# Kernel tuning notes

Hardware: AMD Instinct MI355X
Metric: run time of the kernel (lower is better)

The kernel has to match this reference:

```python
import jax, jax.numpy as jnp
import numpy as np

N, E = 100000, 1600000
NFEAT, NHID, NCLASS, NLAYER = 128, 128, 40, 3


def _glorot(key, shape):
    fan_in, fan_out = shape[0], shape[1]
    lim = float(np.sqrt(6.0 / (fan_in + fan_out)))
    return jax.random.uniform(key, shape, jnp.float32, -lim, lim)


def setup_inputs() -> dict:
    key = jax.random.key(0)
    ks = jax.random.split(key, 12)
    x = jax.random.normal(ks[0], (N, NFEAT), jnp.float32)
    src = jax.random.randint(ks[1], (E,), 0, N, jnp.int32)
    dst = jax.random.randint(ks[2], (E,), 0, N, jnp.int32)
    W1 = _glorot(ks[3], (NFEAT, NHID)); b1 = jnp.zeros((NHID,), jnp.float32)
    W2 = _glorot(ks[4], (NHID, NHID)); b2 = jnp.zeros((NHID,), jnp.float32)
    Wg = jnp.stack([_glorot(ks[5 + l], (NHID, NHID)) for l in range(NLAYER)])  # [L,H,H]
    bg = jnp.zeros((NLAYER, NHID), jnp.float32)
    Wc = _glorot(ks[5 + NLAYER], (NHID, NCLASS)); bc = jnp.zeros((NCLASS,), jnp.float32)
    return {"x": x, "src": src, "dst": dst, "W1": W1, "b1": b1, "W2": W2,
            "b2": b2, "Wg": Wg, "bg": bg, "Wc": Wc, "bc": bc}


def _graph_conv(h, src, dst, W, b, out_norm, in_norm):
    # DGL GraphConv norm='both': scale by src out-deg^{-1/2}, sum-aggregate,
    # scale by dst in-deg^{-1/2}, then linear (in_feats == out_feats -> W after agg).
    h = h * out_norm[:, None]
    agg = jax.ops.segment_sum(h[src], dst, num_segments=N)
    return (agg * in_norm[:, None]) @ W + b


def reference(x, src, dst, W1, b1, W2, b2, Wg, bg, Wc, bc):
    ones = jnp.ones((E,), jnp.float32)
    out_deg = jnp.clip(jax.ops.segment_sum(ones, src, num_segments=N), 1.0)
    in_deg = jnp.clip(jax.ops.segment_sum(ones, dst, num_segments=N), 1.0)
    out_norm = jax.lax.rsqrt(out_deg)
    in_norm = jax.lax.rsqrt(in_deg)

    h = x @ W1 + b1            # feature1
    h = h @ W2 + b2            # feature2
    for l in range(NLAYER):    # stacked GraphConv + ReLU (dropout is identity in eval)
        h = _graph_conv(h, src, dst, Wg[l], bg[l], out_norm, in_norm)
        h = jax.nn.relu(h)
    return h @ Wc + bc         # classifier
```

## Files before the change

### kernel.cpp

```cpp
#include <hip/hip_runtime.h>
#include <hip/hip_fp16.h>
#include <cstdint>
#include <cstddef>

constexpr int NN  = 100000;
constexpr int EE  = 1600000;
constexpr int HID = 128;
constexpr int NBUK = (NN + 511) / 512;
constexpr int BLKE = 2048;
constexpr int NBE  = (EE + BLKE - 1) / BLKE;
constexpr int MH   = NBUK * NBE;
constexpr int NSC  = (MH + 1023) / 1024;

typedef float f32x4_t __attribute__((ext_vector_type(4)));
typedef short bf16x8_t __attribute__((ext_vector_type(8)));

static __device__ __forceinline__ short f2bf(float f) {
    union { float f; unsigned u; } x; x.f = f;
    unsigned r = x.u + 0x7FFF + ((x.u >> 16) & 1);
    return (short)(r >> 16);
}
static __device__ __forceinline__ float bf2f(short b) {
    union { unsigned u; float f; } x; x.u = ((unsigned)(unsigned short)b) << 16;
    return x.f;
}

__global__ __launch_bounds__(256) void bh_both_k(const int* __restrict__ src, const int* __restrict__ dst,
                                                 int* __restrict__ bh_d, int* __restrict__ bh_s) {
    __shared__ int hd[NBUK], hs[NBUK];
    int blk = blockIdx.x, t = threadIdx.x;
    for (int i = t; i < NBUK; i += 256) { hd[i] = 0; hs[i] = 0; }
    __syncthreads();
    int e0 = blk * BLKE, e1 = min(e0 + BLKE, EE);
    for (int e = e0 + t; e < e1; e += 256) {
        atomicAdd(&hd[dst[e] >> 9], 1);
        atomicAdd(&hs[src[e] >> 9], 1);
    }
    __syncthreads();
    for (int i = t; i < NBUK; i += 256) {
        bh_d[i * NBE + blk] = hd[i];
        bh_s[i * NBE + blk] = hs[i];
    }
}

__global__ __launch_bounds__(256) void scan_sum_k(const int* __restrict__ in, int* __restrict__ bsum, int n) {
    __shared__ int sc[256];
    int b = blockIdx.x, t = threadIdx.x;
    int base = b * 1024 + t * 4;
    int s = 0;
#pragma unroll
    for (int j = 0; j < 4; j++) { int idx = base + j; s += (idx < n) ? in[idx] : 0; }
    sc[t] = s; __syncthreads();
    for (int off = 128; off > 0; off >>= 1) {
        if (t < off) sc[t] += sc[t + off];
        __syncthreads();
    }
    if (t == 0) bsum[b] = sc[0];
}

__global__ void scan_top_k(const int* __restrict__ bsum, int* __restrict__ boff, int nb) {
    __shared__ int sc[256];
    int t = threadIdx.x;
    int v = (t < nb) ? bsum[t] : 0;
    sc[t] = v; __syncthreads();
    for (int off = 1; off < 256; off <<= 1) {
        int u = (t >= off) ? sc[t - off] : 0;
        __syncthreads();
        sc[t] += u;
        __syncthreads();
    }
    if (t < nb) boff[t] = sc[t] - v;
}

__global__ __launch_bounds__(256) void scan_chunk_k(const int* __restrict__ in, const int* __restrict__ boff,
                                                    int* __restrict__ out, int n) {
    __shared__ int sc[256];
    int b = blockIdx.x, t = threadIdx.x;
    int base = b * 1024 + t * 4;
    int c[4];
#pragma unroll
    for (int j = 0; j < 4; j++) { int idx = base + j; c[j] = (idx < n) ? in[idx] : 0; }
    int s = c[0] + c[1] + c[2] + c[3];
    sc[t] = s; __syncthreads();
    for (int off = 1; off < 256; off <<= 1) {
        int v = (t >= off) ? sc[t - off] : 0;
        __syncthreads();
        sc[t] += v;
        __syncthreads();
    }
    int excl = sc[t] - s + boff[b];
#pragma unroll
    for (int j = 0; j < 4; j++) {
        int idx = base + j;
        if (idx < n) out[idx] = excl;
        excl += c[j];
    }
}

__global__ __launch_bounds__(256) void scatter_both_k(const int* __restrict__ src, const int* __restrict__ dst,
                                                      const int* __restrict__ off_d, const int* __restrict__ off_s,
                                                      int2* __restrict__ pairs, int* __restrict__ ssorted) {
    __shared__ int cd[NBUK], cs[NBUK];
    int blk = blockIdx.x, t = threadIdx.x;
    for (int i = t; i < NBUK; i += 256) {
        cd[i] = off_d[i * NBE + blk];
        cs[i] = off_s[i * NBE + blk];
    }
    __syncthreads();
    int e0 = blk * BLKE, e1 = min(e0 + BLKE, EE);
    for (int e = e0 + t; e < e1; e += 256) {
        int d = dst[e], s = src[e];
        int pd = atomicAdd(&cd[d >> 9], 1);
        pairs[pd] = make_int2(d, s);
        int ps = atomicAdd(&cs[s >> 9], 1);
        ssorted[ps] = s;
    }
}

__global__ __launch_bounds__(256) void bucket_csr_k(const int2* __restrict__ pairs, const int* __restrict__ off_d,
                                                    int* __restrict__ rowptr, int* __restrict__ col,
                                                    float* __restrict__ inorm) {
    __shared__ int hist[512];
    __shared__ int excl[512];
    __shared__ int psum[256];
    int b = blockIdx.x, t = threadIdx.x;
    int base = off_d[b * NBE];
    int endv = (b == NBUK - 1) ? EE : off_d[(b + 1) * NBE];
    hist[t] = 0; hist[t + 256] = 0;
    __syncthreads();
    for (int i = base + t; i < endv; i += 256) atomicAdd(&hist[pairs[i].x & 511], 1);
    __syncthreads();
    int p0 = hist[2 * t], p1 = hist[2 * t + 1];
    int ps = p0 + p1;
    psum[t] = ps; __syncthreads();
    for (int off = 1; off < 256; off <<= 1) {
        int u = (t >= off) ? psum[t - off] : 0;
        __syncthreads();
        psum[t] += u;
        __syncthreads();
    }
    int pex = psum[t] - ps;
    excl[2 * t] = pex; excl[2 * t + 1] = pex + p0;
    __syncthreads();
    int n0 = b * 512;
#pragma unroll
    for (int j = 0; j < 2; j++) {
        int i = 2 * t + j, node = n0 + i;
        if (node < NN) {
            rowptr[node] = base + excl[i];
            int c = hist[i]; if (c < 1) c = 1;
            inorm[node] = rsqrtf((float)c);
        }
    }
    if (b == NBUK - 1 && t == 0) rowptr[NN] = EE;
    __syncthreads();
    for (int i = base + t; i < endv; i += 256) {
        int2 p = pairs[i];
        int pos = base + atomicAdd(&excl[p.x & 511], 1);
        col[pos] = p.y;
    }
}

__global__ __launch_bounds__(256) void bucket_ocnt_k(const int* __restrict__ ssorted, const int* __restrict__ off_s,
                                                     float* __restrict__ onorm) {
    __shared__ int hist[512];
    int b = blockIdx.x, t = threadIdx.x;
    int base = off_s[b * NBE];
    int endv = (b == NBUK - 1) ? EE : off_s[(b + 1) * NBE];
    hist[t] = 0; hist[t + 256] = 0;
    __syncthreads();
    for (int i = base + t; i < endv; i += 256) atomicAdd(&hist[ssorted[i] & 511], 1);
    __syncthreads();
#pragma unroll
    for (int j = 0; j < 2; j++) {
        int i = t + j * 256, node = b * 512 + i;
        if (node < NN) {
            int c = hist[i]; if (c < 1) c = 1;
            onorm[node] = rsqrtf((float)c);
        }
    }
}

__global__ __launch_bounds__(256) void agg_k(const float4* __restrict__ h16, const int* __restrict__ rowptr,
                                             const int* __restrict__ col, float4* __restrict__ out) {
    int w = (int)((blockIdx.x * 256 + threadIdx.x) >> 6);
    if (w >= NN) return;
    int lane = threadIdx.x & 63;
    int q   = lane >> 4;
    int l16 = lane & 15;
    int beg = rowptr[w], end = rowptr[w + 1];
    float acc[8];
#pragma unroll
    for (int j = 0; j < 8; j++) acc[j] = 0.f;

    union HU { float4 f4; __half2 h2[4]; };
    int i = beg + q;
    for (; i + 12 < end; i += 16) {
        int s0 = col[i], s1 = col[i + 4], s2 = col[i + 8], s3 = col[i + 12];
        HU u0, u1, u2, u3;
        u0.f4 = h16[(size_t)s0 * 16 + l16];
        u1.f4 = h16[(size_t)s1 * 16 + l16];
        u2.f4 = h16[(size_t)s2 * 16 + l16];
        u3.f4 = h16[(size_t)s3 * 16 + l16];
#pragma unroll
        for (int p = 0; p < 4; p++) {
            float2 a = __half22float2(u0.h2[p]);
            float2 b = __half22float2(u1.h2[p]);
            float2 c = __half22float2(u2.h2[p]);
            float2 d = __half22float2(u3.h2[p]);
            acc[2 * p]     += (a.x + b.x) + (c.x + d.x);
            acc[2 * p + 1] += (a.y + b.y) + (c.y + d.y);
        }
    }
    for (; i < end; i += 4) {
        int s = col[i];
        HU u; u.f4 = h16[(size_t)s * 16 + l16];
#pragma unroll
        for (int p = 0; p < 4; p++) {
            float2 a = __half22float2(u.h2[p]);
            acc[2 * p]     += a.x;
            acc[2 * p + 1] += a.y;
        }
    }
#pragma unroll
    for (int m = 16; m <= 32; m <<= 1)
#pragma unroll
        for (int j = 0; j < 8; j++) acc[j] += __shfl_xor(acc[j], m);
    if (q == 0) {
        float4 o0, o1;
        o0.x = acc[0]; o0.y = acc[1]; o0.z = acc[2]; o0.w = acc[3];
        o1.x = acc[4]; o1.y = acc[5]; o1.z = acc[6]; o1.w = acc[7];
        out[(size_t)w * 32 + l16 * 2]     = o0;
        out[(size_t)w * 32 + l16 * 2 + 1] = o1;
    }
}

template <int NT, bool RELU, bool INSCALE, bool OUTSCALE, bool OUTHALF>
__global__ __launch_bounds__(256) void mfma_gemm_k(
    const float* __restrict__ in, const float* __restrict__ inscale,
    const float* __restrict__ W, const float* __restrict__ bias,
    void* __restrict__ outp, const float* __restrict__ outscale,
    int nrows, int ncols, int ngroups) {

    __shared__ short Bh[NT * 2048];
    __shared__ short Bl[NT * 2048];

    const int t = threadIdx.x;

    if constexpr (NT == 8) {
        for (int j = 0; j < 16; j++) {
            int fi = (j * 256 + t) * 4;
            int k = fi >> 7, n0 = fi & 127;
            float4 wv = *(const float4*)(W + fi);
            float wa[4] = {wv.x, wv.y, wv.z, wv.w};
#pragma unroll
            for (int c = 0; c < 4; c++) {
                int n = n0 + c;
                int nt = n >> 4, kblk = k >> 5, ksub = k & 31;
                int lane_ = ((ksub >> 3) << 4) | (n & 15);
                int sidx = ((nt * 4 + kblk) * 64 + lane_) * 8 + (ksub & 7);
                short hi = f2bf(wa[c]);
                short lo = f2bf(wa[c] - bf2f(hi));
                Bh[sidx] = hi; Bl[sidx] = lo;
            }
        }
    } else {
        for (int idx = t; idx < 128 * 64; idx += 256) {
            int k = idx >> 6, n = idx & 63;
            if (n < NT * 16) {
                float w = (n < 40) ? W[k * 40 + n] : 0.f;
                int nt = n >> 4, kblk = k >> 5, ksub = k & 31;
                int lane_ = ((ksub >> 3) << 4) | (n & 15);
                int sidx = ((nt * 4 + kblk) * 64 + lane_) * 8 + (ksub & 7);
                short hi = f2bf(w);
                short lo = f2bf(w - bf2f(hi));
                Bh[sidx] = hi; Bl[sidx] = lo;
            }
        }
    }
    __syncthreads();

    const int wave = t >> 6;
    const int lane = t & 63;
    const int m    = lane & 15;
    const int kq   = lane >> 4;

    for (int g = blockIdx.x; g < ngroups; g += gridDim.x) {
        int grow0 = g * 64 + wave * 16;
        int row   = grow0 + m;
        bool rv   = row < nrows;

        bf16x8_t Ah[4], Al[4];
        float s = 1.f;
        if (INSCALE && rv) s = inscale[row];
#pragma unroll
        for (int kb = 0; kb < 4; kb++) {
            const float* ap = in + (size_t)row * 128 + kb * 32 + kq * 8;
            float4 p0, p1;
            if (rv) { p0 = *(const float4*)ap; p1 = *(const float4*)(ap + 4); }
            else    { p0 = make_float4(0,0,0,0); p1 = make_float4(0,0,0,0); }
            float av[8] = {p0.x, p0.y, p0.z, p0.w, p1.x, p1.y, p1.z, p1.w};
#pragma unroll
            for (int j = 0; j < 8; j++) {
                float v = INSCALE ? av[j] * s : av[j];
                short hi = f2bf(v);
                Ah[kb][j] = hi;
                Al[kb][j] = f2bf(v - bf2f(hi));
            }
        }

        int crow0 = grow0 + kq * 4;
        float osr[4];
#pragma unroll
        for (int r = 0; r < 4; r++) {
            int crow = crow0 + r;
            osr[r] = (OUTSCALE && crow < nrows) ? outscale[crow] : 1.f;
        }

#pragma unroll
        for (int nt = 0; nt < NT; nt++) {
            f32x4_t acc = {0.f, 0.f, 0.f, 0.f};
#pragma unroll
            for (int kb = 0; kb < 4; kb++) {
                const bf16x8_t bh = *(const bf16x8_t*)&Bh[((nt * 4 + kb) * 64 + lane) * 8];
                const bf16x8_t bl = *(const bf16x8_t*)&Bl[((nt * 4 + kb) * 64 + lane) * 8];
                acc = __builtin_amdgcn_mfma_f32_16x16x32_bf16(Ah[kb], bh, acc, 0, 0, 0);
                acc = __builtin_amdgcn_mfma_f32_16x16x32_bf16(Al[kb], bh, acc, 0, 0, 0);
                acc = __builtin_amdgcn_mfma_f32_16x16x32_bf16(Ah[kb], bl, acc, 0, 0, 0);
            }
            int ccol = nt * 16 + m;
            bool cv = (NT == 8) ? true : (ccol < ncols);
            float bv = cv ? bias[ccol] : 0.f;
#pragma unroll
            for (int r = 0; r < 4; r++) {
                int crow = crow0 + r;
                if (crow < nrows && cv) {
                    float v = acc[r] + bv;
                    if (RELU) v = fmaxf(v, 0.f);
                    v *= osr[r];
                    if (OUTHALF) ((__half*)outp)[(size_t)crow * ncols + ccol] = __float2half_rn(v);
                    else         ((float*)outp)[(size_t)crow * ncols + ccol] = v;
                }
            }
        }
    }
}

extern "C" void kernel_launch(void* const* d_in, const int* in_sizes, int n_in,
                              void* d_out, int out_size, void* d_ws, size_t ws_size,
                              hipStream_t stream) {
    const float* x   = (const float*)d_in[0];
    const int*   src = (const int*)d_in[1];
    const int*   dst = (const int*)d_in[2];
    const float* W1  = (const float*)d_in[3];
    const float* b1  = (const float*)d_in[4];
    const float* W2  = (const float*)d_in[5];
    const float* b2  = (const float*)d_in[6];
    const float* Wg  = (const float*)d_in[7];
    const float* bg  = (const float*)d_in[8];
    const float* Wc  = (const float*)d_in[9];
    const float* bc  = (const float*)d_in[10];
    float* out = (float*)d_out;

    char* ws = (char*)d_ws;
    size_t off = 0;
    auto alloc = [&](size_t bytes) -> void* {
        void* p = ws + off;
        off += (bytes + 255) & ~(size_t)255;
        return p;
    };
    float*  h0     = (float*)alloc((size_t)NN * HID * 4);
    float*  h1     = (float*)alloc((size_t)NN * HID * 4);
    __half* h16    = (__half*)alloc((size_t)NN * HID * 2);
    float*  onorm  = (float*)alloc((size_t)NN * 4);
    float*  inorm  = (float*)alloc((size_t)NN * 4);
    int*    rowptr = (int*)alloc((size_t)(NN + 1) * 4);
    int*    col    = (int*)alloc((size_t)EE * 4);
    int*    bh_d   = (int*)alloc((size_t)MH * 4);
    int*    bh_s   = (int*)alloc((size_t)MH * 4);
    int*    off_d  = (int*)alloc((size_t)MH * 4);
    int*    off_s  = (int*)alloc((size_t)MH * 4);
    int*    bsum   = (int*)alloc((size_t)NSC * 4);
    int*    boff   = (int*)alloc((size_t)NSC * 4);
    int2*  pairs   = (int2*)h0;
    int*   ssorted = (int*)(h0 + (size_t)EE * 2);

    bh_both_k<<<NBE, 256, 0, stream>>>(src, dst, bh_d, bh_s);
    scan_sum_k<<<NSC, 256, 0, stream>>>(bh_d, bsum, MH);
    scan_top_k<<<1, 256, 0, stream>>>(bsum, boff, NSC);
    scan_chunk_k<<<NSC, 256, 0, stream>>>(bh_d, boff, off_d, MH);
    scan_sum_k<<<NSC, 256, 0, stream>>>(bh_s, bsum, MH);
    scan_top_k<<<1, 256, 0, stream>>>(bsum, boff, NSC);
    scan_chunk_k<<<NSC, 256, 0, stream>>>(bh_s, boff, off_s, MH);
    scatter_both_k<<<NBE, 256, 0, stream>>>(src, dst, off_d, off_s, pairs, ssorted);
    bucket_csr_k<<<NBUK, 256, 0, stream>>>(pairs, off_d, rowptr, col, inorm);
    bucket_ocnt_k<<<NBUK, 256, 0, stream>>>(ssorted, off_s, onorm);

    const int ngroups = (NN + 63) / 64;
    const int ggrid   = 512;

    mfma_gemm_k<8, false, false, false, false><<<ggrid, 256, 0, stream>>>(
        x, nullptr, W1, b1, h0, nullptr, NN, 128, ngroups);
    mfma_gemm_k<8, false, false, true, true><<<ggrid, 256, 0, stream>>>(
        h0, nullptr, W2, b2, h16, onorm, NN, 128, ngroups);
    for (int l = 0; l < 3; l++) {
        agg_k<<<(NN * 64 + 255) / 256, 256, 0, stream>>>(
            (const float4*)h16, rowptr, col, (float4*)h0);
        if (l < 2) {
            mfma_gemm_k<8, true, true, true, true><<<ggrid, 256, 0, stream>>>(
                h0, inorm, Wg + (size_t)l * 128 * 128, bg + (size_t)l * 128, h16, onorm, NN, 128, ngroups);
        } else {
            mfma_gemm_k<8, true, true, false, false><<<ggrid, 256, 0, stream>>>(
                h0, inorm, Wg + (size_t)l * 128 * 128, bg + (size_t)l * 128, h1, nullptr, NN, 128, ngroups);
        }
    }
    mfma_gemm_k<3, false, false, false, false><<<ggrid, 256, 0, stream>>>(
        h1, nullptr, Wc, bc, out, nullptr, NN, 40, ngroups);
}
```

Before: 613.6 us.

## Fold W1·W2 into one GEMM and store pre-split bf16 hi/lo activations

Precomputes W12 = W1·W2 and b12 = b1·W2 + b2 so the two feature layers collapse into a single GEMM over x. Activations are now written as bf16 hi/lo pairs: by a new split kernel for x, by the aggregation kernel, and by the last graph-conv GEMM. The GEMMs therefore read ready-made MFMA operands instead of fp32 and no longer split them per tile. The GEMM is restructured to 512 threads, with each wave holding one column tile of B in registers, and the in-norm scale is applied after accumulation. This trades an extra split pass over x and two-array bf16 storage for half the GEMM input bandwidth and one fewer full GEMM. The split now truncates the hi part instead of rounding it.

New measurement: 727.4 us. +18.5%, slower.

```diff
diff --git a/kernel.cpp b/kernel.cpp
--- a/kernel.cpp
+++ b/kernel.cpp
@@ -14,15 +14,13 @@
 
 typedef float f32x4_t __attribute__((ext_vector_type(4)));
 typedef short bf16x8_t __attribute__((ext_vector_type(8)));
-
-static __device__ __forceinline__ short f2bf(float f) {
-    union { float f; unsigned u; } x; x.f = f;
-    unsigned r = x.u + 0x7FFF + ((x.u >> 16) & 1);
-    return (short)(r >> 16);
-}
-static __device__ __forceinline__ float bf2f(short b) {
-    union { unsigned u; float f; } x; x.u = ((unsigned)(unsigned short)b) << 16;
-    return x.f;
+typedef unsigned short u16x8_t __attribute__((ext_vector_type(8)));
+
+static __device__ __forceinline__ void fsplit(float v, unsigned short& hi, unsigned short& lo) {
+    unsigned u = __float_as_uint(v);
+    hi = (unsigned short)(u >> 16);
+    float r = v - __uint_as_float(u & 0xFFFF0000u);
+    lo = (unsigned short)(__float_as_uint(r) >> 16);
 }
 
 __global__ __launch_bounds__(256) void bh_both_k(const int* __restrict__ src, const int* __restrict__ dst,
@@ -181,8 +179,45 @@
     }
 }
 
+__global__ __launch_bounds__(256) void w12_k(const float* __restrict__ W1, const float* __restrict__ W2,
+                                             float* __restrict__ W12) {
+    int idx = blockIdx.x * 256 + threadIdx.x;
+    int i = idx >> 7, j = idx & 127;
+    float a0 = 0.f, a1 = 0.f, a2 = 0.f, a3 = 0.f;
+    for (int k = 0; k < 128; k += 4) {
+        a0 = fmaf(W1[i * 128 + k],     W2[(k)     * 128 + j], a0);
+        a1 = fmaf(W1[i * 128 + k + 1], W2[(k + 1) * 128 + j], a1);
+        a2 = fmaf(W1[i * 128 + k + 2], W2[(k + 2) * 128 + j], a2);
+        a3 = fmaf(W1[i * 128 + k + 3], W2[(k + 3) * 128 + j], a3);
+    }
+    W12[idx] = (a0 + a1) + (a2 + a3);
+}
+
+__global__ void b12_k(const float* __restrict__ b1, const float* __restrict__ W2,
+                      const float* __restrict__ b2, float* __restrict__ b12) {
+    int j = threadIdx.x;
+    if (j < 128) {
+        float acc = b2[j];
+        for (int k = 0; k < 128; k++) acc = fmaf(b1[k], W2[k * 128 + j], acc);
+        b12[j] = acc;
+    }
+}
+
+__global__ __launch_bounds__(256) void split_k(const float* __restrict__ x, unsigned short* __restrict__ hi,
+                                               unsigned short* __restrict__ lo) {
+    int i0 = (blockIdx.x * 256 + threadIdx.x) * 8;
+    float4 a = *(const float4*)(x + i0), b = *(const float4*)(x + i0 + 4);
+    float v[8] = {a.x, a.y, a.z, a.w, b.x, b.y, b.z, b.w};
+    u16x8_t h, l;
+#pragma unroll
+    for (int j = 0; j < 8; j++) { unsigned short hh, ll; fsplit(v[j], hh, ll); h[j] = hh; l[j] = ll; }
+    *(u16x8_t*)(hi + i0) = h;
+    *(u16x8_t*)(lo + i0) = l;
+}
+
 __global__ __launch_bounds__(256) void agg_k(const float4* __restrict__ h16, const int* __restrict__ rowptr,
-                                             const int* __restrict__ col, float4* __restrict__ out) {
+                                             const int* __restrict__ col,
+                                             unsigned short* __restrict__ ahi, unsigned short* __restrict__ alo) {
     int w = (int)((blockIdx.x * 256 + threadIdx.x) >> 6);
     if (w >= NN) return;
     int lane = threadIdx.x & 63;
@@ -223,123 +258,103 @@
         }
     }
 #pragma unroll
-    for (int m = 16; m <= 32; m <<= 1)
-#pragma unroll
-        for (int j = 0; j < 8; j++) acc[j] += __shfl_xor(acc[j], m);
+    for (int mm = 16; mm <= 32; mm <<= 1)
+#pragma unroll
+        for (int j = 0; j < 8; j++) acc[j] += __shfl_xor(acc[j], mm);
     if (q == 0) {
-        float4 o0, o1;
-        o0.x = acc[0]; o0.y = acc[1]; o0.z = acc[2]; o0.w = acc[3];
-        o1.x = acc[4]; o1.y = acc[5]; o1.z = acc[6]; o1.w = acc[7];
-        out[(size_t)w * 32 + l16 * 2]     = o0;
-        out[(size_t)w * 32 + l16 * 2 + 1] = o1;
-    }
-}
-
-template <int NT, bool RELU, bool INSCALE, bool OUTSCALE, bool OUTHALF>
-__global__ __launch_bounds__(256) void mfma_gemm_k(
-    const float* __restrict__ in, const float* __restrict__ inscale,
-    const float* __restrict__ W, const float* __restrict__ bias,
-    void* __restrict__ outp, const float* __restrict__ outscale,
+        u16x8_t h, l;
+#pragma unroll
+        for (int j = 0; j < 8; j++) { unsigned short hh, ll; fsplit(acc[j], hh, ll); h[j] = hh; l[j] = ll; }
+        *(u16x8_t*)(ahi + (size_t)w * 128 + l16 * 8) = h;
+        *(u16x8_t*)(alo + (size_t)w * 128 + l16 * 8) = l;
+    }
+}
+
+template <int NT, bool RELU, bool INSC, int OM, bool OUTSC>
+__global__ __launch_bounds__(512) void gemm_bs_k(
+    const unsigned short* __restrict__ Ahi, const unsigned short* __restrict__ Alo,
+    const float* __restrict__ insc,
+    const float* __restrict__ W, int wld, const float* __restrict__ bias,
+    void* __restrict__ o1, void* __restrict__ o2, const float* __restrict__ outsc,
     int nrows, int ncols, int ngroups) {
 
     __shared__ short Bh[NT * 2048];
     __shared__ short Bl[NT * 2048];
-
     const int t = threadIdx.x;
-
-    if constexpr (NT == 8) {
-        for (int j = 0; j < 16; j++) {
-            int fi = (j * 256 + t) * 4;
-            int k = fi >> 7, n0 = fi & 127;
-            float4 wv = *(const float4*)(W + fi);
-            float wa[4] = {wv.x, wv.y, wv.z, wv.w};
-#pragma unroll
-            for (int c = 0; c < 4; c++) {
-                int n = n0 + c;
-                int nt = n >> 4, kblk = k >> 5, ksub = k & 31;
-                int lane_ = ((ksub >> 3) << 4) | (n & 15);
-                int sidx = ((nt * 4 + kblk) * 64 + lane_) * 8 + (ksub & 7);
-                short hi = f2bf(wa[c]);
-                short lo = f2bf(wa[c] - bf2f(hi));
-                Bh[sidx] = hi; Bl[sidx] = lo;
+    for (int idx = t; idx < 128 * 128; idx += 512) {
+        int k = idx >> 7, n = idx & 127;
+        if (n < NT * 16) {
+            float wv = (n < ncols) ? W[k * wld + n] : 0.f;
+            unsigned short hh, ll; fsplit(wv, hh, ll);
+            int nt_ = n >> 4, kblk = k >> 5, ksub = k & 31;
+            int lane_ = ((ksub >> 3) << 4) | (n & 15);
+            int sidx = ((nt_ * 4 + kblk) * 64 + lane_) * 8 + (ksub & 7);
+            Bh[sidx] = (short)hh; Bl[sidx] = (short)ll;
+        }
+    }
+    __syncthreads();
+
+    const int wave = t >> 6, lane = t & 63, m = lane & 15, kq = lane >> 4;
+    int nt, rg0, nrg;
+    bool active;
+    if (NT == 8) { nt = wave; rg0 = 0; nrg = 4; active = true; }
+    else         { nt = wave % 3; rg0 = (wave / 3) * 2; nrg = 2; active = wave < 6; }
+    if (!active) return;
+
+    bf16x8_t bh[4], bl[4];
+#pragma unroll
+    for (int kb = 0; kb < 4; kb++) {
+        bh[kb] = *(const bf16x8_t*)&Bh[((nt * 4 + kb) * 64 + lane) * 8];
+        bl[kb] = *(const bf16x8_t*)&Bl[((nt * 4 + kb) * 64 + lane) * 8];
+    }
+    const int ccol = nt * 16 + m;
+    const bool cv = (NT == 8) || (ccol < ncols);
+    const float bv = cv ? bias[ccol] : 0.f;
+
+    for (int g = blockIdx.x; g < ngroups; g += gridDim.x) {
+        for (int rgi = 0; rgi < nrg; rgi++) {
+            int rg = rg0 + rgi;
+            int row0 = g * 64 + rg * 16;
+            int row = row0 + m;
+            bool rv = row < nrows;
+            bf16x8_t ah[4], al[4];
+#pragma unroll
+            for (int kb = 0; kb < 4; kb++) {
+                if (rv) {
+                    const size_t o = (size_t)row * 128 + kb * 32 + kq * 8;
+                    ah[kb] = *(const bf16x8_t*)(Ahi + o);
+                    al[kb] = *(const bf16x8_t*)(Alo + o);
+                } else {
+                    ah[kb] = (bf16x8_t){0,0,0,0,0,0,0,0};
+                    al[kb] = (bf16x8_t){0,0,0,0,0,0,0,0};
+                }
             }
-        }
-    } else {
-        for (int idx = t; idx < 128 * 64; idx += 256) {
-            int k = idx >> 6, n = idx & 63;
-            if (n < NT * 16) {
-                float w = (n < 40) ? W[k * 40 + n] : 0.f;
-                int nt = n >> 4, kblk = k >> 5, ksub = k & 31;
-                int lane_ = ((ksub >> 3) << 4) | (n & 15);
-                int sidx = ((nt * 4 + kblk) * 64 + lane_) * 8 + (ksub & 7);
-                short hi = f2bf(w);
-                short lo = f2bf(w - bf2f(hi));
-                Bh[sidx] = hi; Bl[sidx] = lo;
+            f32x4_t acc = {0.f, 0.f, 0.f, 0.f};
+#pragma unroll
+            for (int kb = 0; kb < 4; kb++) {
+                acc = __builtin_amdgcn_mfma_f32_16x16x32_bf16(ah[kb], bh[kb], acc, 0, 0, 0);
+                acc = __builtin_amdgcn_mfma_f32_16x16x32_bf16(al[kb], bh[kb], acc, 0, 0, 0);
+                acc = __builtin_amdgcn_mfma_f32_16x16x32_bf16(ah[kb], bl[kb], acc, 0, 0, 0);
             }
-        }
-    }
-    __syncthreads();
-
-    const int wave = t >> 6;
-    const int lane = t & 63;
-    const int m    = lane & 15;
-    const int kq   = lane >> 4;
-
-    for (int g = blockIdx.x; g < ngroups; g += gridDim.x) {
-        int grow0 = g * 64 + wave * 16;
-        int row   = grow0 + m;
-        bool rv   = row < nrows;
-
-        bf16x8_t Ah[4], Al[4];
-        float s = 1.f;
-        if (INSCALE && rv) s = inscale[row];
-#pragma unroll
-        for (int kb = 0; kb < 4; kb++) {
-            const float* ap = in + (size_t)row * 128 + kb * 32 + kq * 8;
-            float4 p0, p1;
-            if (rv) { p0 = *(const float4*)ap; p1 = *(const float4*)(ap + 4); }
-            else    { p0 = make_float4(0,0,0,0); p1 = make_float4(0,0,0,0); }
-            float av[8] = {p0.x, p0.y, p0.z, p0.w, p1.x, p1.y, p1.z, p1.w};
-#pragma unroll
-            for (int j = 0; j < 8; j++) {
-                float v = INSCALE ? av[j] * s : av[j];
-                short hi = f2bf(v);
-                Ah[kb][j] = hi;
-                Al[kb][j] = f2bf(v - bf2f(hi));
-            }
-        }
-
-        int crow0 = grow0 + kq * 4;
-        float osr[4];
-#pragma unroll
-        for (int r = 0; r < 4; r++) {
-            int crow = crow0 + r;
-            osr[r] = (OUTSCALE && crow < nrows) ? outscale[crow] : 1.f;
-        }
-
-#pragma unroll
-        for (int nt = 0; nt < NT; nt++) {
-            f32x4_t acc = {0.f, 0.f, 0.f, 0.f};
-#pragma unroll
-            for (int kb = 0; kb < 4; kb++) {
-                const bf16x8_t bh = *(const bf16x8_t*)&Bh[((nt * 4 + kb) * 64 + lane) * 8];
-                const bf16x8_t bl = *(const bf16x8_t*)&Bl[((nt * 4 + kb) * 64 + lane) * 8];
-                acc = __builtin_amdgcn_mfma_f32_16x16x32_bf16(Ah[kb], bh, acc, 0, 0, 0);
-                acc = __builtin_amdgcn_mfma_f32_16x16x32_bf16(Al[kb], bh, acc, 0, 0, 0);
-                acc = __builtin_amdgcn_mfma_f32_16x16x32_bf16(Ah[kb], bl, acc, 0, 0, 0);
-            }
-            int ccol = nt * 16 + m;
-            bool cv = (NT == 8) ? true : (ccol < ncols);
-            float bv = cv ? bias[ccol] : 0.f;
+            int crow0 = row0 + kq * 4;
 #pragma unroll
             for (int r = 0; r < 4; r++) {
                 int crow = crow0 + r;
                 if (crow < nrows && cv) {
-                    float v = acc[r] + bv;
+                    float v = acc[r];
+                    if (INSC) v *= insc[crow];
+                    v += bv;
                     if (RELU) v = fmaxf(v, 0.f);
-                    v *= osr[r];
-                    if (OUTHALF) ((__half*)outp)[(size_t)crow * ncols + ccol] = __float2half_rn(v);
-                    else         ((float*)outp)[(size_t)crow * ncols + ccol] = v;
+                    if (OUTSC) v *= outsc[crow];
+                    if (OM == 0) {
+                        ((float*)o1)[(size_t)crow * ncols + ccol] = v;
+                    } else if (OM == 1) {
+                        ((__half*)o1)[(size_t)crow * 128 + ccol] = __float2half_rn(v);
+                    } else {
+                        unsigned short hh, ll; fsplit(v, hh, ll);
+                        ((unsigned short*)o1)[(size_t)crow * 128 + ccol] = hh;
+                        ((unsigned short*)o2)[(size_t)crow * 128 + ccol] = ll;
+                    }
                 }
             }
         }
@@ -369,9 +384,13 @@
         off += (bytes + 255) & ~(size_t)255;
         return p;
     };
-    float*  h0     = (float*)alloc((size_t)NN * HID * 4);
-    float*  h1     = (float*)alloc((size_t)NN * HID * 4);
-    __half* h16    = (__half*)alloc((size_t)NN * HID * 2);
+    __half*         h16   = (__half*)alloc((size_t)NN * HID * 2);
+    unsigned short* ahi   = (unsigned short*)alloc((size_t)NN * HID * 2);
+    unsigned short* alo   = (unsigned short*)alloc((size_t)NN * HID * 2);
+    unsigned short* xhi   = (unsigned short*)alloc((size_t)NN * HID * 2);
+    unsigned short* xlo   = (unsigned short*)alloc((size_t)NN * HID * 2);
+    float*  W12    = (float*)alloc(128 * 128 * 4);
+    float*  b12    = (float*)alloc(128 * 4);
     float*  onorm  = (float*)alloc((size_t)NN * 4);
     float*  inorm  = (float*)alloc((size_t)NN * 4);
     int*    rowptr = (int*)alloc((size_t)(NN + 1) * 4);
@@ -382,8 +401,8 @@
     int*    off_s  = (int*)alloc((size_t)MH * 4);
     int*    bsum   = (int*)alloc((size_t)NSC * 4);
     int*    boff   = (int*)alloc((size_t)NSC * 4);
-    int2*  pairs   = (int2*)h0;
-    int*   ssorted = (int*)(h0 + (size_t)EE * 2);
+    int2* pairs   = (int2*)h16;
+    int*  ssorted = (int*)((char*)h16 + (size_t)EE * 8);
 
     bh_both_k<<<NBE, 256, 0, stream>>>(src, dst, bh_d, bh_s);
     scan_sum_k<<<NSC, 256, 0, stream>>>(bh_d, bsum, MH);
@@ -396,24 +415,28 @@
     bucket_csr_k<<<NBUK, 256, 0, stream>>>(pairs, off_d, rowptr, col, inorm);
     bucket_ocnt_k<<<NBUK, 256, 0, stream>>>(ssorted, off_s, onorm);
 
+    w12_k<<<64, 256, 0, stream>>>(W1, W2, W12);
+    b12_k<<<1, 128, 0, stream>>>(b1, W2, b2, b12);
+    split_k<<<(NN * HID / 8 + 255) / 256, 256, 0, stream>>>(x, xhi, xlo);
+
     const int ngroups = (NN + 63) / 64;
     const int ggrid   = 512;
 
-    mfma_gemm_k<8, false, false, false, false><<<ggrid, 256, 0, stream>>>(
-        x, nullptr, W1, b1, h0, nullptr, NN, 128, ngroups);
-    mfma_gemm_k<8, false, false, true, true><<<ggrid, 256, 0, stream>>>(
-        h0, nullptr, W2, b2, h16, onorm, NN, 128, ngroups);
+    gemm_bs_k<8, false, false, 1, true><<<ggrid, 512, 0, stream>>>(
+        xhi, xlo, nullptr, W12, 128, b12, h16, nullptr, onorm, NN, 128, ngroups);
     for (int l = 0; l < 3; l++) {
         agg_k<<<(NN * 64 + 255) / 256, 256, 0, stream>>>(
-            (const float4*)h16, rowptr, col, (float4*)h0);
+            (const float4*)h16, rowptr, col, ahi, alo);
         if (l < 2) {
-            mfma_gemm_k<8, true, true, true, true><<<ggrid, 256, 0, stream>>>(
-                h0, inorm, Wg + (size_t)l * 128 * 128, bg + (size_t)l * 128, h16, onorm, NN, 128, ngroups);
+            gemm_bs_k<8, true, true, 1, true><<<ggrid, 512, 0, stream>>>(
+                ahi, alo, inorm, Wg + (size_t)l * 128 * 128, 128, bg + (size_t)l * 128,
+                h16, nullptr, onorm, NN, 128, ngroups);
         } else {
-            mfma_gemm_k<8, true, true, false, false><<<ggrid, 256, 0, stream>>>(
-                h0, inorm, Wg + (size_t)l * 128 * 128, bg + (size_t)l * 128, h1, nullptr, NN, 128, ngroups);
-        }
-    }
-    mfma_gemm_k<3, false, false, false, false><<<ggrid, 256, 0, stream>>>(
-        h1, nullptr, Wc, bc, out, nullptr, NN, 40, ngroups);
-}
+            gemm_bs_k<8, true, true, 2, false><<<ggrid, 512, 0, stream>>>(
+                ahi, alo, inorm, Wg + (size_t)l * 128 * 128, 128, bg + (size_t)l * 128,
+                xhi, xlo, nullptr, NN, 128, ngroups);
+        }
+    }
+    gemm_bs_k<3, false, false, 0, false><<<ggrid, 512, 0, stream>>>(
+        xhi, xlo, nullptr, Wc, 40, bc, out, nullptr, nullptr, NN, 40, ngroups);
+}
```

## Fold W1·W2 into one weight and switch GEMMs to two-term fp16 MFMA

Applied to the files above, without the earlier changes.

The two chained linear layers are precomputed into one combined weight and bias by small device kernels, which removes a full N×128 GEMM pass and its intermediate write and read. The GEMM kernel moves from a three-MFMA bf16 hi/lo split to an fp16 hi/lo split of the activation only, with a single fp16 weight. That halves weight LDS and cuts MFMA count per tile. The input scale is now applied after accumulation, bias is hoisted out of the group loop, and the grid is one block per row group. Precision drops somewhat because the weights are rounded to plain fp16 and the activation is split at fp16 range.

After: 738.4 us. +20.3%, slower.

```diff
diff --git a/kernel.cpp b/kernel.cpp
--- a/kernel.cpp
+++ b/kernel.cpp
@@ -12,18 +12,8 @@
 constexpr int MH   = NBUK * NBE;
 constexpr int NSC  = (MH + 1023) / 1024;
 
-typedef float f32x4_t __attribute__((ext_vector_type(4)));
-typedef short bf16x8_t __attribute__((ext_vector_type(8)));
-
-static __device__ __forceinline__ short f2bf(float f) {
-    union { float f; unsigned u; } x; x.f = f;
-    unsigned r = x.u + 0x7FFF + ((x.u >> 16) & 1);
-    return (short)(r >> 16);
-}
-static __device__ __forceinline__ float bf2f(short b) {
-    union { unsigned u; float f; } x; x.u = ((unsigned)(unsigned short)b) << 16;
-    return x.f;
-}
+typedef float    f32x4 __attribute__((ext_vector_type(4)));
+typedef _Float16 f16x8 __attribute__((ext_vector_type(8)));
 
 __global__ __launch_bounds__(256) void bh_both_k(const int* __restrict__ src, const int* __restrict__ dst,
                                                  int* __restrict__ bh_d, int* __restrict__ bh_s) {
@@ -181,6 +171,30 @@
     }
 }
 
+__global__ __launch_bounds__(256) void w12_k(const float* __restrict__ W1, const float* __restrict__ W2,
+                                             float* __restrict__ W12) {
+    int idx = blockIdx.x * 256 + threadIdx.x;
+    int i = idx >> 7, j = idx & 127;
+    float a0 = 0.f, a1 = 0.f, a2 = 0.f, a3 = 0.f;
+    for (int k = 0; k < 128; k += 4) {
+        a0 = fmaf(W1[i * 128 + k],     W2[(k)     * 128 + j], a0);
+        a1 = fmaf(W1[i * 128 + k + 1], W2[(k + 1) * 128 + j], a1);
+        a2 = fmaf(W1[i * 128 + k + 2], W2[(k + 2) * 128 + j], a2);
+        a3 = fmaf(W1[i * 128 + k + 3], W2[(k + 3) * 128 + j], a3);
+    }
+    W12[idx] = (a0 + a1) + (a2 + a3);
+}
+
+__global__ void b12_k(const float* __restrict__ b1, const float* __restrict__ W2,
+                      const float* __restrict__ b2, float* __restrict__ b12) {
+    int j = threadIdx.x;
+    if (j < 128) {
+        float acc = b2[j];
+        for (int k = 0; k < 128; k++) acc = fmaf(b1[k], W2[k * 128 + j], acc);
+        b12[j] = acc;
+    }
+}
+
 __global__ __launch_bounds__(256) void agg_k(const float4* __restrict__ h16, const int* __restrict__ rowptr,
                                              const int* __restrict__ col, float4* __restrict__ out) {
     int w = (int)((blockIdx.x * 256 + threadIdx.x) >> 6);
@@ -223,9 +237,9 @@
         }
     }
 #pragma unroll
-    for (int m = 16; m <= 32; m <<= 1)
-#pragma unroll
-        for (int j = 0; j < 8; j++) acc[j] += __shfl_xor(acc[j], m);
+    for (int mm = 16; mm <= 32; mm <<= 1)
+#pragma unroll
+        for (int j = 0; j < 8; j++) acc[j] += __shfl_xor(acc[j], mm);
     if (q == 0) {
         float4 o0, o1;
         o0.x = acc[0]; o0.y = acc[1]; o0.z = acc[2]; o0.w = acc[3];
@@ -235,16 +249,14 @@
     }
 }
 
-template <int NT, bool RELU, bool INSCALE, bool OUTSCALE, bool OUTHALF>
-__global__ __launch_bounds__(256) void mfma_gemm_k(
-    const float* __restrict__ in, const float* __restrict__ inscale,
+template <int NT, bool RELU, bool INSC, bool OUTSC, bool OUTHALF>
+__global__ __launch_bounds__(256, 4) void gemm_h2_k(
+    const float* __restrict__ in, const float* __restrict__ insc,
     const float* __restrict__ W, const float* __restrict__ bias,
-    void* __restrict__ outp, const float* __restrict__ outscale,
+    void* __restrict__ outp, const float* __restrict__ outsc,
     int nrows, int ncols, int ngroups) {
 
-    __shared__ short Bh[NT * 2048];
-    __shared__ short Bl[NT * 2048];
-
+    __shared__ __align__(16) _Float16 Bs[NT * 2048];
     const int t = threadIdx.x;
 
     if constexpr (NT == 8) {
@@ -259,9 +271,7 @@
                 int nt = n >> 4, kblk = k >> 5, ksub = k & 31;
                 int lane_ = ((ksub >> 3) << 4) | (n & 15);
                 int sidx = ((nt * 4 + kblk) * 64 + lane_) * 8 + (ksub & 7);
-                short hi = f2bf(wa[c]);
-                short lo = f2bf(wa[c] - bf2f(hi));
-                Bh[sidx] = hi; Bl[sidx] = lo;
+                Bs[sidx] = (_Float16)wa[c];
             }
         }
     } else {
@@ -272,9 +282,7 @@
                 int nt = n >> 4, kblk = k >> 5, ksub = k & 31;
                 int lane_ = ((ksub >> 3) << 4) | (n & 15);
                 int sidx = ((nt * 4 + kblk) * 64 + lane_) * 8 + (ksub & 7);
-                short hi = f2bf(w);
-                short lo = f2bf(w - bf2f(hi));
-                Bh[sidx] = hi; Bl[sidx] = lo;
+                Bs[sidx] = (_Float16)w;
             }
         }
     }
@@ -285,14 +293,19 @@
     const int m    = lane & 15;
     const int kq   = lane >> 4;
 
+    float bv[NT];
+#pragma unroll
+    for (int nt = 0; nt < NT; nt++) {
+        int ccol = nt * 16 + m;
+        bv[nt] = (ccol < ncols) ? bias[ccol] : 0.f;
+    }
+
     for (int g = blockIdx.x; g < ngroups; g += gridDim.x) {
         int grow0 = g * 64 + wave * 16;
         int row   = grow0 + m;
         bool rv   = row < nrows;
 
-        bf16x8_t Ah[4], Al[4];
-        float s = 1.f;
-        if (INSCALE && rv) s = inscale[row];
+        f16x8 Ah[4], Al[4];
 #pragma unroll
         for (int kb = 0; kb < 4; kb++) {
             const float* ap = in + (size_t)row * 128 + kb * 32 + kq * 8;
@@ -302,42 +315,42 @@
             float av[8] = {p0.x, p0.y, p0.z, p0.w, p1.x, p1.y, p1.z, p1.w};
 #pragma unroll
             for (int j = 0; j < 8; j++) {
-                float v = INSCALE ? av[j] * s : av[j];
-                short hi = f2bf(v);
-                Ah[kb][j] = hi;
-                Al[kb][j] = f2bf(v - bf2f(hi));
+                _Float16 hh = (_Float16)av[j];
+                Ah[kb][j] = hh;
+                Al[kb][j] = (_Float16)(av[j] - (float)hh);
             }
         }
 
         int crow0 = grow0 + kq * 4;
-        float osr[4];
+        float isr[4], osr[4];
 #pragma unroll
         for (int r = 0; r < 4; r++) {
             int crow = crow0 + r;
-            osr[r] = (OUTSCALE && crow < nrows) ? outscale[crow] : 1.f;
+            bool cva = crow < nrows;
+            isr[r] = (INSC && cva) ? insc[crow] : 1.f;
+            osr[r] = (OUTSC && cva) ? outsc[crow] : 1.f;
         }
 
 #pragma unroll
         for (int nt = 0; nt < NT; nt++) {
-            f32x4_t acc = {0.f, 0.f, 0.f, 0.f};
+            f32x4 acc = {0.f, 0.f, 0.f, 0.f};
 #pragma unroll
             for (int kb = 0; kb < 4; kb++) {
-                const bf16x8_t bh = *(const bf16x8_t*)&Bh[((nt * 4 + kb) * 64 + lane) * 8];
-                const bf16x8_t bl = *(const bf16x8_t*)&Bl[((nt * 4 + kb) * 64 + lane) * 8];
-                acc = __builtin_amdgcn_mfma_f32_16x16x32_bf16(Ah[kb], bh, acc, 0, 0, 0);
-                acc = __builtin_amdgcn_mfma_f32_16x16x32_bf16(Al[kb], bh, acc, 0, 0, 0);
-                acc = __builtin_amdgcn_mfma_f32_16x16x32_bf16(Ah[kb], bl, acc, 0, 0, 0);
+                const f16x8 b = *(const f16x8*)&Bs[((nt * 4 + kb) * 64 + lane) * 8];
+                acc = __builtin_amdgcn_mfma_f32_16x16x32_f16(Ah[kb], b, acc, 0, 0, 0);
+                acc = __builtin_amdgcn_mfma_f32_16x16x32_f16(Al[kb], b, acc, 0, 0, 0);
             }
             int ccol = nt * 16 + m;
             bool cv = (NT == 8) ? true : (ccol < ncols);
-            float bv = cv ? bias[ccol] : 0.f;
 #pragma unroll
             for (int r = 0; r < 4; r++) {
                 int crow = crow0 + r;
                 if (crow < nrows && cv) {
-                    float v = acc[r] + bv;
+                    float v = acc[r];
+                    if (INSC) v *= isr[r];
+                    v += bv[nt];
                     if (RELU) v = fmaxf(v, 0.f);
-                    v *= osr[r];
+                    if (OUTSC) v *= osr[r];
                     if (OUTHALF) ((__half*)outp)[(size_t)crow * ncols + ccol] = __float2half_rn(v);
                     else         ((float*)outp)[(size_t)crow * ncols + ccol] = v;
                 }
@@ -372,6 +385,8 @@
     float*  h0     = (float*)alloc((size_t)NN * HID * 4);
     float*  h1     = (float*)alloc((size_t)NN * HID * 4);
     __half* h16    = (__half*)alloc((size_t)NN * HID * 2);
+    float*  W12    = (float*)alloc(128 * 128 * 4);
+    float*  b12    = (float*)alloc(128 * 4);
     float*  onorm  = (float*)alloc((size_t)NN * 4);
     float*  inorm  = (float*)alloc((size_t)NN * 4);
     int*    rowptr = (int*)alloc((size_t)(NN + 1) * 4);
@@ -382,8 +397,8 @@
     int*    off_s  = (int*)alloc((size_t)MH * 4);
     int*    bsum   = (int*)alloc((size_t)NSC * 4);
     int*    boff   = (int*)alloc((size_t)NSC * 4);
-    int2*  pairs   = (int2*)h0;
-    int*   ssorted = (int*)(h0 + (size_t)EE * 2);
+    int2* pairs   = (int2*)h0;
+    int*  ssorted = (int*)((char*)h0 + (size_t)EE * 8);
 
     bh_both_k<<<NBE, 256, 0, stream>>>(src, dst, bh_d, bh_s);
     scan_sum_k<<<NSC, 256, 0, stream>>>(bh_d, bsum, MH);
@@ -396,24 +411,24 @@
     bucket_csr_k<<<NBUK, 256, 0, stream>>>(pairs, off_d, rowptr, col, inorm);
     bucket_ocnt_k<<<NBUK, 256, 0, stream>>>(ssorted, off_s, onorm);
 
+    w12_k<<<64, 256, 0, stream>>>(W1, W2, W12);
+    b12_k<<<1, 128, 0, stream>>>(b1, W2, b2, b12);
+
     const int ngroups = (NN + 63) / 64;
-    const int ggrid   = 512;
-
-    mfma_gemm_k<8, false, false, false, false><<<ggrid, 256, 0, stream>>>(
-        x, nullptr, W1, b1, h0, nullptr, NN, 128, ngroups);
-    mfma_gemm_k<8, false, false, true, true><<<ggrid, 256, 0, stream>>>(
-        h0, nullptr, W2, b2, h16, onorm, NN, 128, ngroups);
+
+    gemm_h2_k<8, false, false, true, true><<<ngroups, 256, 0, stream>>>(
+        x, nullptr, W12, b12, h16, onorm, NN, 128, ngroups);
     for (int l = 0; l < 3; l++) {
         agg_k<<<(NN * 64 + 255) / 256, 256, 0, stream>>>(
             (const float4*)h16, rowptr, col, (float4*)h0);
         if (l < 2) {
-            mfma_gemm_k<8, true, true, true, true><<<ggrid, 256, 0, stream>>>(
+            gemm_h2_k<8, true, true, true, true><<<ngroups, 256, 0, stream>>>(
                 h0, inorm, Wg + (size_t)l * 128 * 128, bg + (size_t)l * 128, h16, onorm, NN, 128, ngroups);
         } else {
-            mfma_gemm_k<8, true, true, false, false><<<ggrid, 256, 0, stream>>>(
+            gemm_h2_k<8, true, true, false, false><<<ngroups, 256, 0, stream>>>(
                 h0, inorm, Wg + (size_t)l * 128 * 128, bg + (size_t)l * 128, h1, nullptr, NN, 128, ngroups);
         }
     }
-    mfma_gemm_k<3, false, false, false, false><<<ggrid, 256, 0, stream>>>(
+    gemm_h2_k<3, false, false, false, false><<<ngroups, 256, 0, stream>>>(
         h1, nullptr, Wc, bc, out, nullptr, NN, 40, ngroups);
 }
```
